# Optimization experiments

Hardware: AMD Instinct MI355X
Metric: run time of the kernel (lower is better)

The kernel has to match this reference:

```python
import jax, jax.numpy as jnp
import numpy as np

DIM_K = 64
DIM_V = 64
MODEL_DIM = 1024


def setup_inputs() -> dict:
    key = jax.random.key(0)
    ks = jax.random.split(key, 9)
    B, T, C = 4, 4096, MODEL_DIM
    scale = 1.0 / np.sqrt(C)
    return {
        "Q": jax.random.normal(ks[0], (B, T, C), dtype=jnp.float32),
        "K": jax.random.normal(ks[1], (B, T, C), dtype=jnp.float32),
        "V": jax.random.normal(ks[2], (B, T, C), dtype=jnp.float32),
        "Wq": jax.random.normal(ks[3], (C, DIM_K), dtype=jnp.float32) * scale,
        "bq": jax.random.normal(ks[4], (DIM_K,), dtype=jnp.float32) * 0.02,
        "Wk": jax.random.normal(ks[5], (C, DIM_K), dtype=jnp.float32) * scale,
        "bk": jax.random.normal(ks[6], (DIM_K,), dtype=jnp.float32) * 0.02,
        "Wv": jax.random.normal(ks[7], (C, DIM_V), dtype=jnp.float32) * scale,
        "bv": jax.random.normal(ks[8], (DIM_V,), dtype=jnp.float32) * 0.02,
    }


def reference(Q, K, V, Wq, bq, Wk, bk, Wv, bv):
    # Linear projections: [B,T,C] @ [C,dk] -> [B,T,dk]
    q = jnp.einsum("btc,cd->btd", Q, Wq) + bq
    k = jnp.einsum("btc,cd->btd", K, Wk) + bk
    v = jnp.einsum("btc,cd->btd", V, Wv) + bv
    T = q.shape[1]
    # Scaled dot-product scores [B,T,T], causal mask, softmax (dropout p=0 -> identity)
    scores = jnp.einsum("bqd,bkd->bqk", q, k) / jnp.sqrt(jnp.float32(DIM_K))
    causal = jnp.tril(jnp.ones((T, T), dtype=bool))
    scores = jnp.where(causal, scores, -jnp.inf)
    weights = jax.nn.softmax(scores, axis=-1)
    return jnp.einsum("bqk,bkd->bqd", weights, v)
```

## Files before the change

### kernel.cpp

```cpp
#include <hip/hip_runtime.h>
#include <hip/hip_bf16.h>
#include <cstdint>
#include <cstddef>


typedef __attribute__((ext_vector_type(8))) short short8;
typedef __attribute__((ext_vector_type(4))) float f32x4;
typedef __attribute__((ext_vector_type(4))) unsigned int uint4v;
typedef __attribute__((ext_vector_type(4))) unsigned short ushort4v;

#define MFMA16x16x32(A,B,C) __builtin_amdgcn_mfma_f32_16x16x32_bf16((A),(B),(C),0,0,0)

static __device__ __forceinline__ unsigned pack2_bf16(float f0, float f1){
  unsigned u0 = __builtin_bit_cast(unsigned, f0) + 0x8000u;
  unsigned u1 = __builtin_bit_cast(unsigned, f1) + 0x8000u;
  return __builtin_amdgcn_perm(u1, u0, 0x07060302u);
}
static __device__ __forceinline__ unsigned short bf16u(float f){
  return (unsigned short)((__builtin_bit_cast(unsigned, f) + 0x8000u) >> 16);
}
static __device__ __forceinline__ short8 cvt8(f32x4 a, f32x4 b){
  union { unsigned u[4]; short8 s; } r;
  r.u[0] = pack2_bf16(a[0], a[1]);
  r.u[1] = pack2_bf16(a[2], a[3]);
  r.u[2] = pack2_bf16(b[0], b[1]);
  r.u[3] = pack2_bf16(b[2], b[3]);
  return r.s;
}
static __device__ __forceinline__ float fast_exp2(float x){
  float r; asm("v_exp_f32 %0, %1" : "=v"(r) : "v"(x)); return r;
}
static __device__ __forceinline__ float fast_rcp(float x){
  float r; asm("v_rcp_f32 %0, %1" : "=v"(r) : "v"(x)); return r;
}

__global__ __launch_bounds__(256) void pack_w(
    const float* __restrict__ Wq, const float* __restrict__ Wk,
    const float* __restrict__ Wv, unsigned short* __restrict__ Wp,
    float* __restrict__ out, float* __restrict__ Lbuf)
{
  int t = blockIdx.x * 256 + threadIdx.x;
  if (t < 24576){
    int lane = t & 63, nf = (t >> 6) & 3, cc = (t >> 8) & 31, p = t >> 13;
    int qd = lane >> 4, l = lane & 15;
    const float* W = (p == 0) ? Wq : ((p == 1) ? Wk : Wv);
    const float* src = W + (size_t)(cc * 32 + qd * 8) * 64 + nf * 16 + l;
    uint4v u;
    #pragma unroll
    for (int j = 0; j < 4; ++j)
      u[j] = pack2_bf16(src[(2 * j) * 64], src[(2 * j + 1) * 64]);
    *(uint4v*)(Wp + (size_t)t * 8) = u;
  }
  const f32x4 z = (f32x4){0.f, 0.f, 0.f, 0.f};
  f32x4* o4 = (f32x4*)out;
  f32x4* l4 = (f32x4*)Lbuf;
  for (int i = t; i < 262144 + 4096; i += 65536){
    if (i < 262144) o4[i] = z;
    else l4[i - 262144] = z;
  }
}

__global__ __launch_bounds__(256) void proj_gemm(
    const float* __restrict__ Qx, const float* __restrict__ Kx, const float* __restrict__ Vx,
    const float* __restrict__ bqp, const float* __restrict__ bkp, const float* __restrict__ bvp,
    const unsigned short* __restrict__ Wp,
    unsigned short* __restrict__ qb, unsigned short* __restrict__ kb,
    unsigned short* __restrict__ vt)
{
  const int tid = threadIdx.x;
  const int lane = tid & 63, wid = tid >> 6;
  const int qd = lane >> 4, l = lane & 15;
  const int p = blockIdx.y;
  const float* X = (p == 0) ? Qx : ((p == 1) ? Kx : Vx);
  const float* bias = (p == 0) ? bqp : ((p == 1) ? bkp : bvp);
  const unsigned short* W = Wp + (size_t)p * 65536;

  const int row0 = blockIdx.x * 64 + wid * 16;
  const float* xa = X + (size_t)(row0 + l) * 1024 + qd * 8;
  const unsigned short* wb = W + (size_t)lane * 8;

  f32x4 acc[4];
  #pragma unroll
  for (int nf = 0; nf < 4; ++nf) acc[nf] = (f32x4){0.f, 0.f, 0.f, 0.f};

  #pragma unroll 4
  for (int cc = 0; cc < 32; ++cc){
    f32x4 al = *(const f32x4*)(xa + cc * 32);
    f32x4 ah = *(const f32x4*)(xa + cc * 32 + 4);
    const unsigned short* wc = wb + (size_t)cc * 2048;
    short8 b0 = *(const short8*)(wc);
    short8 b1 = *(const short8*)(wc + 512);
    short8 b2 = *(const short8*)(wc + 1024);
    short8 b3 = *(const short8*)(wc + 1536);
    short8 a = cvt8(al, ah);
    acc[0] = MFMA16x16x32(a, b0, acc[0]);
    acc[1] = MFMA16x16x32(a, b1, acc[1]);
    acc[2] = MFMA16x16x32(a, b2, acc[2]);
    acc[3] = MFMA16x16x32(a, b3, acc[3]);
  }

  if (p == 2){
    int tg = row0 + qd * 4;
    int b = tg >> 12, tl = tg & 4095;
    #pragma unroll
    for (int nf = 0; nf < 4; ++nf){
      float bb = bias[nf * 16 + l];
      ushort4v pk;
      #pragma unroll
      for (int r = 0; r < 4; ++r) pk[r] = bf16u(acc[nf][r] + bb);
      *(ushort4v*)(vt + ((size_t)b * 64 + nf * 16 + l) * 4096 + tl) = pk;
    }
  } else {
    unsigned short* o = (p == 0) ? qb : kb;
    #pragma unroll
    for (int nf = 0; nf < 4; ++nf){
      float bb = bias[nf * 16 + l];
      #pragma unroll
      for (int r = 0; r < 4; ++r){
        int row = row0 + qd * 4 + r;
        o[(size_t)row * 64 + nf * 16 + l] = bf16u(acc[nf][r] + bb);
      }
    }
  }
}

#define K1 0.18033688011112042f

__global__ __launch_bounds__(256) void flash_split(
    const unsigned short* __restrict__ qb, const unsigned short* __restrict__ kb,
    const unsigned short* __restrict__ vt, float* __restrict__ out,
    float* __restrict__ Lbuf)
{
  __shared__ unsigned short pbuf[4][16 * 40];
  const int tid = threadIdx.x;
  const int lane = tid & 63, wid = tid >> 6;
  const int qd = lane >> 4, l = lane & 15;
  const int batch = wid;

  int j = 1151 - (int)blockIdx.x;
  int g = 0;
  while (j >= 16 * (g + 1) * (g + 2)) ++g;
  int r0 = j - 16 * g * (g + 1);
  int tq = r0 / (g + 1);
  const int t = 32 * g + tq;
  const int s = r0 - tq * (g + 1);
  const int q0 = t * 16;
  const int kvstart = s * 512;
  const int kvend = min(512 * (s + 1), q0 + 16);

  const unsigned short* qrow = qb + ((size_t)(batch * 4096 + q0 + l)) * 64 + qd * 8;
  short8 Qf0 = *(const short8*)(qrow);
  short8 Qf1 = *(const short8*)(qrow + 32);

  const unsigned short* kbase = kb + (size_t)batch * 4096 * 64;
  const unsigned short* vbase = vt + (size_t)batch * 64 * 4096;

  const f32x4 Zc = (f32x4){0.f, 0.f, 0.f, 0.f};
  f32x4 Oc[4] = {Zc, Zc, Zc, Zc};
  f32x4 Lacc = Zc;
  short8 onesf;
  #pragma unroll
  for (int i = 0; i < 8; ++i) onesf[i] = (short)0x3F80;

  unsigned short* pw = &pbuf[wid][0];
  unsigned short* pwr = pw + qd * 160 + l;
  const unsigned short* prd = pw + l * 40 + qd * 8;

#define FLASH_BODY(CUR, NXT, KV0)                                              \
  do {                                                                         \
    int kvn_ = (KV0) + 32; if (kvn_ >= kvend) kvn_ = kvstart;                  \
    const unsigned short* kp_ = kbase + (size_t)(kvn_ + l) * 64 + qd * 8;      \
    NXT[0] = *(const short8*)(kp_);                                            \
    NXT[1] = *(const short8*)(kp_ + 32);                                       \
    NXT[2] = *(const short8*)(kp_ + 1024);                                     \
    NXT[3] = *(const short8*)(kp_ + 1056);                                     \
    const unsigned short* vp_ = vbase + (size_t)l * 4096 + kvn_ + qd * 8;      \
    NXT[4] = *(const short8*)(vp_);                                            \
    NXT[5] = *(const short8*)(vp_ + 16 * 4096);                                \
    NXT[6] = *(const short8*)(vp_ + 32 * 4096);                                \
    NXT[7] = *(const short8*)(vp_ + 48 * 4096);                                \
    f32x4 s0_ = MFMA16x16x32(Qf0, CUR[0], Zc);                                 \
    s0_ = MFMA16x16x32(Qf1, CUR[1], s0_);                                      \
    f32x4 s1_ = MFMA16x16x32(Qf0, CUR[2], Zc);                                 \
    s1_ = MFMA16x16x32(Qf1, CUR[3], s1_);                                      \
    float p0_[4], p1_[4];                                                      \
    _Pragma("unroll")                                                          \
    for (int r = 0; r < 4; ++r){                                               \
      p0_[r] = fast_exp2(s0_[r] * K1);                                         \
      p1_[r] = fast_exp2(s1_[r] * K1);                                         \
    }                                                                          \
    if ((KV0) + 31 > q0){                                                      \
      _Pragma("unroll")                                                        \
      for (int r = 0; r < 4; ++r){                                             \
        int q_ = q0 + qd * 4 + r;                                              \
        if ((KV0) + l > q_) p0_[r] = 0.f;                                      \
        if ((KV0) + 16 + l > q_) p1_[r] = 0.f;                                 \
      }                                                                        \
    }                                                                          \
    _Pragma("unroll")                                                          \
    for (int r = 0; r < 4; ++r){                                               \
      pwr[r * 40] = bf16u(p0_[r]);                                             \
      pwr[r * 40 + 16] = bf16u(p1_[r]);                                        \
    }                                                                          \
    short8 Pf_ = *(const short8*)(prd);                                        \
    Lacc = MFMA16x16x32(Pf_, onesf, Lacc);                                     \
    Oc[0] = MFMA16x16x32(Pf_, CUR[4], Oc[0]);                                  \
    Oc[1] = MFMA16x16x32(Pf_, CUR[5], Oc[1]);                                  \
    Oc[2] = MFMA16x16x32(Pf_, CUR[6], Oc[2]);                                  \
    Oc[3] = MFMA16x16x32(Pf_, CUR[7], Oc[3]);                                  \
  } while (0)

  short8 bufA[8], bufB[8];
  {
    const unsigned short* kp_ = kbase + (size_t)(kvstart + l) * 64 + qd * 8;
    bufA[0] = *(const short8*)(kp_);
    bufA[1] = *(const short8*)(kp_ + 32);
    bufA[2] = *(const short8*)(kp_ + 1024);
    bufA[3] = *(const short8*)(kp_ + 1056);
    const unsigned short* vp_ = vbase + (size_t)l * 4096 + kvstart + qd * 8;
    bufA[4] = *(const short8*)(vp_);
    bufA[5] = *(const short8*)(vp_ + 16 * 4096);
    bufA[6] = *(const short8*)(vp_ + 32 * 4096);
    bufA[7] = *(const short8*)(vp_ + 48 * 4096);
  }
  int kv0 = kvstart;
  for (;;){
    FLASH_BODY(bufA, bufB, kv0);
    kv0 += 32; if (kv0 >= kvend) break;
    FLASH_BODY(bufB, bufA, kv0);
    kv0 += 32; if (kv0 >= kvend) break;
  }
#undef FLASH_BODY

  float* ob = out + ((size_t)(batch * 4096 + q0 + qd * 4)) * 64 + l;
  #pragma unroll
  for (int nf = 0; nf < 4; ++nf)
    #pragma unroll
    for (int r = 0; r < 4; ++r)
      atomicAdd(&ob[(size_t)r * 64 + nf * 16], Oc[nf][r]);
  if (l == 0){
    float* lb = Lbuf + batch * 4096 + q0 + qd * 4;
    #pragma unroll
    for (int r = 0; r < 4; ++r) atomicAdd(&lb[r], Lacc[r]);
  }
}

__global__ __launch_bounds__(256) void normalize(
    float* __restrict__ out, const float* __restrict__ Lbuf)
{
  int idx = blockIdx.x * 256 + threadIdx.x;
  f32x4 v = ((f32x4*)out)[idx];
  float inv = fast_rcp(Lbuf[idx >> 4]);
  v[0] *= inv; v[1] *= inv; v[2] *= inv; v[3] *= inv;
  ((f32x4*)out)[idx] = v;
}

extern "C" void kernel_launch(void* const* d_in, const int* in_sizes, int n_in,
                              void* d_out, int out_size, void* d_ws, size_t ws_size,
                              hipStream_t stream)
{
  const float* Q  = (const float*)d_in[0];
  const float* K  = (const float*)d_in[1];
  const float* V  = (const float*)d_in[2];
  const float* Wq = (const float*)d_in[3];
  const float* bq = (const float*)d_in[4];
  const float* Wk = (const float*)d_in[5];
  const float* bk = (const float*)d_in[6];
  const float* Wv = (const float*)d_in[7];
  const float* bv = (const float*)d_in[8];
  float* out = (float*)d_out;

  unsigned short* qb   = (unsigned short*)d_ws;
  unsigned short* kbuf = qb + (size_t)16384 * 64;
  unsigned short* vtp  = kbuf + (size_t)16384 * 64;
  unsigned short* Wp   = vtp + (size_t)16384 * 64;
  float* Lbuf = (float*)(Wp + (size_t)3 * 65536);

  pack_w<<<256, 256, 0, stream>>>(Wq, Wk, Wv, Wp, out, Lbuf);
  proj_gemm<<<dim3(256, 3), 256, 0, stream>>>(Q, K, V, bq, bk, bv, Wp, qb, kbuf, vtp);
  flash_split<<<1152, 256, 0, stream>>>(qb, kbuf, vtp, out, Lbuf);
  normalize<<<1024, 256, 0, stream>>>(out, Lbuf);
}
```

Baseline: 300.0 us.

## Share K/V tiles across waves via LDS with async global-to-LDS loads

Restructures the flash kernel so that each block handles 64 queries of a single batch (four waves of 16 rows each), not one 16-row tile per wave across four batches. K and V 64-key tiles are loaded once per block into swizzled, double-buffered LDS using global_load_lds and shared by all four waves. The goal is to cut redundant global/L2 traffic by a factor of four. In exchange it adds block-wide __syncthreads per tile, extra LDS reads, and some idle waves on diagonal tiles.

Result: faster. 253.1 us (-15.6%).

```diff
diff --git a/kernel.cpp b/kernel.cpp
--- a/kernel.cpp
+++ b/kernel.cpp
@@ -8,6 +8,7 @@
 typedef __attribute__((ext_vector_type(4))) float f32x4;
 typedef __attribute__((ext_vector_type(4))) unsigned int uint4v;
 typedef __attribute__((ext_vector_type(4))) unsigned short ushort4v;
+typedef unsigned short ushort;
 
 #define MFMA16x16x32(A,B,C) __builtin_amdgcn_mfma_f32_16x16x32_bf16((A),(B),(C),0,0,0)
 
@@ -32,6 +33,11 @@
 }
 static __device__ __forceinline__ float fast_rcp(float x){
   float r; asm("v_rcp_f32 %0, %1" : "=v"(r) : "v"(x)); return r;
+}
+static __device__ __forceinline__ void gl_lds16(const ushort* g, ushort* l){
+  __builtin_amdgcn_global_load_lds(
+      (const __attribute__((address_space(1))) void*)g,
+      (__attribute__((address_space(3))) void*)l, 16, 0, 0);
 }
 
 __global__ __launch_bounds__(256) void pack_w(
@@ -127,33 +133,38 @@
 #define K1 0.18033688011112042f
 
 __global__ __launch_bounds__(256) void flash_split(
-    const unsigned short* __restrict__ qb, const unsigned short* __restrict__ kb,
-    const unsigned short* __restrict__ vt, float* __restrict__ out,
+    const ushort* __restrict__ qb, const ushort* __restrict__ kb,
+    const ushort* __restrict__ vt, float* __restrict__ out,
     float* __restrict__ Lbuf)
 {
-  __shared__ unsigned short pbuf[4][16 * 40];
+  __shared__ ushort Ks[2][4096];
+  __shared__ ushort Vs[2][4096];
+  __shared__ ushort pbuf[4][16 * 40];
+
   const int tid = threadIdx.x;
   const int lane = tid & 63, wid = tid >> 6;
   const int qd = lane >> 4, l = lane & 15;
-  const int batch = wid;
-
-  int j = 1151 - (int)blockIdx.x;
+  const int lw = l & 7;
+
+  int bidx = (int)blockIdx.x;
+  const int batch = bidx & 3;
+  int j = 287 - (bidx >> 2);
   int g = 0;
-  while (j >= 16 * (g + 1) * (g + 2)) ++g;
-  int r0 = j - 16 * g * (g + 1);
-  int tq = r0 / (g + 1);
-  const int t = 32 * g + tq;
-  const int s = r0 - tq * (g + 1);
-  const int q0 = t * 16;
+  while (j >= 4 * (g + 1) * (g + 2)) ++g;
+  int j2 = j - 4 * g * (g + 1);
+  int tq = j2 / (g + 1);
+  int s = j2 - tq * (g + 1);
+  const int q0b = (8 * g + tq) * 64;
   const int kvstart = s * 512;
-  const int kvend = min(512 * (s + 1), q0 + 16);
-
-  const unsigned short* qrow = qb + ((size_t)(batch * 4096 + q0 + l)) * 64 + qd * 8;
+  const int kvend = min(kvstart + 512, q0b + 64);
+  const int q0w = q0b + wid * 16;
+
+  const ushort* kbB = kb + (size_t)batch * 262144;
+  const ushort* vtB = vt + (size_t)batch * 262144;
+
+  const ushort* qrow = qb + ((size_t)(batch * 4096 + q0w + l)) * 64 + qd * 8;
   short8 Qf0 = *(const short8*)(qrow);
   short8 Qf1 = *(const short8*)(qrow + 32);
-
-  const unsigned short* kbase = kb + (size_t)batch * 4096 * 64;
-  const unsigned short* vbase = vt + (size_t)batch * 64 * 4096;
 
   const f32x4 Zc = (f32x4){0.f, 0.f, 0.f, 0.f};
   f32x4 Oc[4] = {Zc, Zc, Zc, Zc};
@@ -162,84 +173,89 @@
   #pragma unroll
   for (int i = 0; i < 8; ++i) onesf[i] = (short)0x3F80;
 
-  unsigned short* pw = &pbuf[wid][0];
-  unsigned short* pwr = pw + qd * 160 + l;
-  const unsigned short* prd = pw + l * 40 + qd * 8;
-
-#define FLASH_BODY(CUR, NXT, KV0)                                              \
-  do {                                                                         \
-    int kvn_ = (KV0) + 32; if (kvn_ >= kvend) kvn_ = kvstart;                  \
-    const unsigned short* kp_ = kbase + (size_t)(kvn_ + l) * 64 + qd * 8;      \
-    NXT[0] = *(const short8*)(kp_);                                            \
-    NXT[1] = *(const short8*)(kp_ + 32);                                       \
-    NXT[2] = *(const short8*)(kp_ + 1024);                                     \
-    NXT[3] = *(const short8*)(kp_ + 1056);                                     \
-    const unsigned short* vp_ = vbase + (size_t)l * 4096 + kvn_ + qd * 8;      \
-    NXT[4] = *(const short8*)(vp_);                                            \
-    NXT[5] = *(const short8*)(vp_ + 16 * 4096);                                \
-    NXT[6] = *(const short8*)(vp_ + 32 * 4096);                                \
-    NXT[7] = *(const short8*)(vp_ + 48 * 4096);                                \
-    f32x4 s0_ = MFMA16x16x32(Qf0, CUR[0], Zc);                                 \
-    s0_ = MFMA16x16x32(Qf1, CUR[1], s0_);                                      \
-    f32x4 s1_ = MFMA16x16x32(Qf0, CUR[2], Zc);                                 \
-    s1_ = MFMA16x16x32(Qf1, CUR[3], s1_);                                      \
-    float p0_[4], p1_[4];                                                      \
-    _Pragma("unroll")                                                          \
-    for (int r = 0; r < 4; ++r){                                               \
-      p0_[r] = fast_exp2(s0_[r] * K1);                                         \
-      p1_[r] = fast_exp2(s1_[r] * K1);                                         \
-    }                                                                          \
-    if ((KV0) + 31 > q0){                                                      \
+  ushort* pw = &pbuf[wid][0];
+  ushort* pwr = pw + qd * 160 + l;
+  const ushort* prd = pw + l * 40 + qd * 8;
+
+#define STAGE(BB, KVC) do{                                                     \
+    int r8_ = lane >> 3, sw_ = ((lane & 7) ^ r8_) << 3;                        \
+    int rA_ = wid * 8 + r8_;                                                   \
+    const ushort* gk_ = kbB + (size_t)((KVC) + rA_) * 64 + sw_;                \
+    gl_lds16(gk_,            &Ks[BB][wid * 512]);                              \
+    gl_lds16(gk_ + 32 * 64,  &Ks[BB][2048 + wid * 512]);                       \
+    const ushort* gv_ = vtB + (size_t)rA_ * 4096 + (KVC) + sw_;                \
+    gl_lds16(gv_,              &Vs[BB][wid * 512]);                            \
+    gl_lds16(gv_ + 32 * 4096,  &Vs[BB][2048 + wid * 512]);                     \
+  } while (0)
+
+#define CHUNK(BB, ROFF, KVG) do{                                               \
+    if ((KVG) < q0w + 16){                                                     \
+      const ushort* KsB_ = &Ks[BB][0];                                         \
+      const ushort* VsB_ = &Vs[BB][0];                                         \
+      short8 k0_ = *(const short8*)(KsB_ + (l + (ROFF)) * 64 + ((qd ^ lw) << 3));        \
+      short8 k1_ = *(const short8*)(KsB_ + (l + (ROFF)) * 64 + (((qd + 4) ^ lw) << 3));  \
+      short8 k2_ = *(const short8*)(KsB_ + (l + 16 + (ROFF)) * 64 + ((qd ^ lw) << 3));   \
+      short8 k3_ = *(const short8*)(KsB_ + (l + 16 + (ROFF)) * 64 + (((qd + 4) ^ lw) << 3)); \
+      f32x4 s0_ = MFMA16x16x32(Qf0, k0_, Zc);                                  \
+      s0_ = MFMA16x16x32(Qf1, k1_, s0_);                                       \
+      f32x4 s1_ = MFMA16x16x32(Qf0, k2_, Zc);                                  \
+      s1_ = MFMA16x16x32(Qf1, k3_, s1_);                                       \
+      float p0_[4], p1_[4];                                                    \
       _Pragma("unroll")                                                        \
       for (int r = 0; r < 4; ++r){                                             \
-        int q_ = q0 + qd * 4 + r;                                              \
-        if ((KV0) + l > q_) p0_[r] = 0.f;                                      \
-        if ((KV0) + 16 + l > q_) p1_[r] = 0.f;                                 \
+        p0_[r] = fast_exp2(s0_[r] * K1);                                       \
+        p1_[r] = fast_exp2(s1_[r] * K1);                                       \
       }                                                                        \
+      if ((KVG) + 31 > q0w){                                                   \
+        _Pragma("unroll")                                                      \
+        for (int r = 0; r < 4; ++r){                                           \
+          int q_ = q0w + qd * 4 + r;                                           \
+          if ((KVG) + l > q_) p0_[r] = 0.f;                                    \
+          if ((KVG) + 16 + l > q_) p1_[r] = 0.f;                               \
+        }                                                                      \
+      }                                                                        \
+      _Pragma("unroll")                                                        \
+      for (int r = 0; r < 4; ++r){                                             \
+        pwr[r * 40] = bf16u(p0_[r]);                                           \
+        pwr[r * 40 + 16] = bf16u(p1_[r]);                                      \
+      }                                                                        \
+      short8 Pf_ = *(const short8*)(prd);                                      \
+      int vs_ = ((qd + ((ROFF) >> 3)) ^ lw) << 3;                              \
+      short8 v0_ = *(const short8*)(VsB_ + (l     ) * 64 + vs_);               \
+      short8 v1_ = *(const short8*)(VsB_ + (l + 16) * 64 + vs_);               \
+      short8 v2_ = *(const short8*)(VsB_ + (l + 32) * 64 + vs_);               \
+      short8 v3_ = *(const short8*)(VsB_ + (l + 48) * 64 + vs_);               \
+      Lacc = MFMA16x16x32(Pf_, onesf, Lacc);                                   \
+      Oc[0] = MFMA16x16x32(Pf_, v0_, Oc[0]);                                   \
+      Oc[1] = MFMA16x16x32(Pf_, v1_, Oc[1]);                                   \
+      Oc[2] = MFMA16x16x32(Pf_, v2_, Oc[2]);                                   \
+      Oc[3] = MFMA16x16x32(Pf_, v3_, Oc[3]);                                   \
     }                                                                          \
-    _Pragma("unroll")                                                          \
-    for (int r = 0; r < 4; ++r){                                               \
-      pwr[r * 40] = bf16u(p0_[r]);                                             \
-      pwr[r * 40 + 16] = bf16u(p1_[r]);                                        \
-    }                                                                          \
-    short8 Pf_ = *(const short8*)(prd);                                        \
-    Lacc = MFMA16x16x32(Pf_, onesf, Lacc);                                     \
-    Oc[0] = MFMA16x16x32(Pf_, CUR[4], Oc[0]);                                  \
-    Oc[1] = MFMA16x16x32(Pf_, CUR[5], Oc[1]);                                  \
-    Oc[2] = MFMA16x16x32(Pf_, CUR[6], Oc[2]);                                  \
-    Oc[3] = MFMA16x16x32(Pf_, CUR[7], Oc[3]);                                  \
   } while (0)
 
-  short8 bufA[8], bufB[8];
-  {
-    const unsigned short* kp_ = kbase + (size_t)(kvstart + l) * 64 + qd * 8;
-    bufA[0] = *(const short8*)(kp_);
-    bufA[1] = *(const short8*)(kp_ + 32);
-    bufA[2] = *(const short8*)(kp_ + 1024);
-    bufA[3] = *(const short8*)(kp_ + 1056);
-    const unsigned short* vp_ = vbase + (size_t)l * 4096 + kvstart + qd * 8;
-    bufA[4] = *(const short8*)(vp_);
-    bufA[5] = *(const short8*)(vp_ + 16 * 4096);
-    bufA[6] = *(const short8*)(vp_ + 32 * 4096);
-    bufA[7] = *(const short8*)(vp_ + 48 * 4096);
-  }
-  int kv0 = kvstart;
-  for (;;){
-    FLASH_BODY(bufA, bufB, kv0);
-    kv0 += 32; if (kv0 >= kvend) break;
-    FLASH_BODY(bufB, bufA, kv0);
-    kv0 += 32; if (kv0 >= kvend) break;
-  }
-#undef FLASH_BODY
-
-  float* ob = out + ((size_t)(batch * 4096 + q0 + qd * 4)) * 64 + l;
+  const int nst = (kvend - kvstart) >> 6;
+  STAGE(0, kvstart);
+  __syncthreads();
+  int kvc = kvstart;
+  for (int it = 0; it < nst; ++it){
+    int bb = it & 1;
+    if (it + 1 < nst) STAGE(bb ^ 1, kvc + 64);
+    CHUNK(bb, 0, kvc);
+    CHUNK(bb, 32, kvc + 32);
+    __syncthreads();
+    kvc += 64;
+  }
+#undef STAGE
+#undef CHUNK
+
+  float* ob = out + ((size_t)(batch * 4096 + q0w + qd * 4)) * 64 + l;
   #pragma unroll
   for (int nf = 0; nf < 4; ++nf)
     #pragma unroll
     for (int r = 0; r < 4; ++r)
       atomicAdd(&ob[(size_t)r * 64 + nf * 16], Oc[nf][r]);
   if (l == 0){
-    float* lb = Lbuf + batch * 4096 + q0 + qd * 4;
+    float* lb = Lbuf + batch * 4096 + q0w + qd * 4;
     #pragma unroll
     for (int r = 0; r < 4; ++r) atomicAdd(&lb[r], Lacc[r]);
   }
```
